# Performance work log

Hardware: AMD Instinct MI355X
Metric: run time of the kernel (lower is better)

Reference implementation:

```python
import jax, jax.numpy as jnp
import numpy as np

C = 512
NH = 8
HD = C // NH              # head dim = 64
TOPK = int(HD * 2 / 3)    # keep top-2/3 entries per attention row (DRSformer-style)


def conv2d(x, w, b, groups=1, pad=0):
    y = jax.lax.conv_general_dilated(
        x, w, window_strides=(1, 1), padding=[(pad, pad), (pad, pad)],
        dimension_numbers=('NCHW', 'OIHW', 'NCHW'), feature_group_count=groups)
    return y + b[None, :, None, None]


def setup_inputs() -> dict:
    key = jax.random.key(0)
    ks = jax.random.split(key, 8)
    s = lambda k, sh, fan: jax.random.normal(k, sh, jnp.float32) * (1.0 / np.sqrt(fan))
    return {
        'x': jax.random.normal(ks[0], (2, C, 128, 128), jnp.float32),
        'w_qkv': s(ks[1], (3 * C, C, 1, 1), C),          # 1x1 conv C -> 3C
        'b_qkv': jnp.zeros((3 * C,), jnp.float32),
        'w_dw': s(ks[2], (3 * C, 1, 3, 3), 9),           # 3x3 depthwise on 3C
        'b_dw': jnp.zeros((3 * C,), jnp.float32),
        'scale': jnp.asarray(HD ** -0.5, jnp.float32),   # learned scalar temperature
        'w_proj': s(ks[3], (C, C, 1, 1), C),             # output 1x1 conv
        'b_proj': jnp.zeros((C,), jnp.float32),
    }


def reference(x, w_qkv, b_qkv, w_dw, b_dw, scale, w_proj, b_proj):
    B, _, H, W = x.shape
    # qkv generator: 1x1 conv then 3x3 depthwise conv (Restormer-style)
    qkv = conv2d(x, w_qkv, b_qkv)
    qkv = conv2d(qkv, w_dw, b_dw, groups=3 * C, pad=1)
    q, k, v = jnp.split(qkv, 3, axis=1)
    # b (nh c) h w -> b nh c (h w)
    rs = lambda t: t.reshape(B, NH, HD, H * W)
    q, k, v = rs(q), rs(k), rs(v)
    # L2-normalize along spatial (token) dim
    q = q / jnp.maximum(jnp.linalg.norm(q, axis=-1, keepdims=True), 1e-12)
    k = k / jnp.maximum(jnp.linalg.norm(k, axis=-1, keepdims=True), 1e-12)
    # transposed (channel) attention: [B, NH, HD, HD]
    att = jnp.einsum('bhcn,bhdn->bhcd', q, k) * scale
    # sparsify: keep top-k per row, mask rest to -inf, then softmax
    thresh = jax.lax.top_k(att, TOPK)[0][..., -1:]
    att = jnp.where(att >= thresh, att, -jnp.inf)
    att = jax.nn.softmax(att, axis=-1)
    out = jnp.einsum('bhcd,bhdn->bhcn', att, v)  # [B, NH, HD, HW]
    out = out.reshape(B, C, H, W)
    return conv2d(out, w_proj, b_proj)
```

## Files before the change

### kernel.cpp

```cpp
#include <hip/hip_runtime.h>

typedef unsigned short u16;
typedef _Float16 f16x8 __attribute__((ext_vector_type(8)));
typedef u16 u16x8 __attribute__((ext_vector_type(8)));
typedef u16 u16x4 __attribute__((ext_vector_type(4)));
typedef float f32x4 __attribute__((ext_vector_type(4)));

#define NTOK 16384
#define CCH 512
#define SXN ((long)CCH * NTOK)

__device__ __forceinline__ float h2f(u16 u) {
  _Float16 h = *(_Float16*)&u; return (float)h;
}
__device__ __forceinline__ u16 f2h(float f) {
  _Float16 h = (_Float16)f; return *(u16*)&h;
}
__device__ __forceinline__ void split2(float v, u16& hi, u16& lo) {
  hi = f2h(v); lo = f2h(v - h2f(hi));
}
__device__ __forceinline__ int swz(int row, int ko) { return ko ^ ((row & 7) << 3); }

__device__ __forceinline__ int k2swz(int r, int x) {
  int s = x >> 2, e = x & 3;
  int ps = (((s >> 2) + r) & 7) | ((s & 3) << 3);
  return r * 128 + (ps << 2) + e;
}

__global__ __launch_bounds__(256) void k0_transpose(
    const float* __restrict__ x, u16* __restrict__ xh) {
  __shared__ float ld[64][65];
  const int t = threadIdx.x;
  const int n0 = blockIdx.x * 64, c0 = blockIdx.y * 64;
#pragma unroll
  for (int j = 0; j < 4; ++j) {
    int idx = t + 256 * j;
    int cl = idx >> 4, ns = (idx & 15) * 4;
    float4 v = *(const float4*)(x + (long)(c0 + cl) * NTOK + n0 + ns);
    ld[cl][ns] = v.x; ld[cl][ns + 1] = v.y; ld[cl][ns + 2] = v.z; ld[cl][ns + 3] = v.w;
  }
  __syncthreads();
#pragma unroll
  for (int j = 0; j < 4; ++j) {
    int idx = t + 256 * j;
    int nl = idx >> 4, cs = (idx & 15) * 4;
    u16x4 h;
#pragma unroll
    for (int e = 0; e < 4; ++e) h[e] = f2h(ld[cs + e][nl]);
    *(u16x4*)(xh + (long)(n0 + nl) * CCH + c0 + cs) = h;
  }
}

__global__ __launch_bounds__(256) void k0_cvt_w(const float* __restrict__ a,
                                                u16* __restrict__ oh,
                                                u16* __restrict__ ol) {
  int i = blockIdx.x * 256 + threadIdx.x;
  const float4 v = ((const float4*)a)[i];
  u16 h0, l0, h1, l1, h2, l2, h3, l3;
  split2(v.x, h0, l0); split2(v.y, h1, l1);
  split2(v.z, h2, l2); split2(v.w, h3, l3);
  ((unsigned long long*)oh)[i] = (unsigned long long)h0 | ((unsigned long long)h1 << 16)
                               | ((unsigned long long)h2 << 32) | ((unsigned long long)h3 << 48);
  ((unsigned long long*)ol)[i] = (unsigned long long)l0 | ((unsigned long long)l1 << 16)
                               | ((unsigned long long)l2 << 32) | ((unsigned long long)l3 << 48);
}

__device__ __forceinline__ void storeC(u16* p, float v) { *p = f2h(v); }
__device__ __forceinline__ void storeC(float* p, float v) { *p = v; }

template <typename OutT, bool BIAS_ROW, int GRP, bool GRP_IS_M>
__global__ __launch_bounds__(256) void gemm_bt(
    const u16* __restrict__ A, const u16* __restrict__ B, OutT* __restrict__ C,
    const float* __restrict__ bias, int ldc) {
  const int K = 512;
  __shared__ __align__(16) u16 lA[128 * 64];
  __shared__ __align__(16) u16 lB[128 * 64];
  const int t = threadIdx.x;
  const int lane = t & 63, w = t >> 6;
  const int wm = w & 1, wn = w >> 1;
  const int fx = blockIdx.x, fy = blockIdx.y;
  const int gg = fy & (GRP - 1);
  const int go = fx + 8 * (fy / GRP);
  const int bm = (GRP_IS_M ? gg : go) * 128;
  const int bn = (GRP_IS_M ? go : gg) * 128;
  const f32x4 zero4 = {0.f, 0.f, 0.f, 0.f};
  f32x4 acc[4][4];
#pragma unroll
  for (int i = 0; i < 4; ++i)
#pragma unroll
    for (int j = 0; j < 4; ++j) acc[i][j] = zero4;

  for (int kt = 0; kt < K; kt += 64) {
    u16x8 ra[4], rb[4];
#pragma unroll
    for (int j = 0; j < 4; ++j) {
      int idx = t + 256 * j;
      int row = idx >> 3, ko = (idx & 7) << 3;
      ra[j] = *(const u16x8*)(A + (long)(bm + row) * K + kt + ko);
      rb[j] = *(const u16x8*)(B + (long)(bn + row) * K + kt + ko);
    }
    __syncthreads();
#pragma unroll
    for (int j = 0; j < 4; ++j) {
      int idx = t + 256 * j;
      int row = idx >> 3, ko = (idx & 7) << 3;
      *(u16x8*)(&lA[row * 64 + swz(row, ko)]) = ra[j];
      *(u16x8*)(&lB[row * 64 + swz(row, ko)]) = rb[j];
    }
    __syncthreads();
#pragma unroll
    for (int kk = 0; kk < 2; ++kk) {
      f16x8 af[4], bfr[4];
#pragma unroll
      for (int f = 0; f < 4; ++f) {
        int ar = wm * 64 + f * 16 + (lane & 15);
        int br = wn * 64 + f * 16 + (lane & 15);
        int ko = kk * 32 + (lane >> 4) * 8;
        af[f]  = *(const f16x8*)(&lA[ar * 64 + swz(ar, ko)]);
        bfr[f] = *(const f16x8*)(&lB[br * 64 + swz(br, ko)]);
      }
#pragma unroll
      for (int i = 0; i < 4; ++i)
#pragma unroll
        for (int jj = 0; jj < 4; ++jj)
          acc[i][jj] = __builtin_amdgcn_mfma_f32_16x16x32_f16(af[i], bfr[jj], acc[i][jj], 0, 0, 0);
    }
  }
#pragma unroll
  for (int i = 0; i < 4; ++i) {
    const int r0 = bm + wm * 64 + i * 16 + (lane >> 4) * 4;
#pragma unroll
    for (int jj = 0; jj < 4; ++jj) {
      const int c0 = bn + wn * 64 + jj * 16 + (lane & 15);
      const float bcol = BIAS_ROW ? 0.f : bias[c0];
#pragma unroll
      for (int r = 0; r < 4; ++r) {
        float v = acc[i][jj][r] + (BIAS_ROW ? bias[r0 + r] : bcol);
        storeC(&C[(long)(r0 + r) * ldc + c0], v);
      }
    }
  }
}

__global__ __launch_bounds__(256) void gemm_split(
    const u16* __restrict__ Ah, const u16* __restrict__ Al,
    const u16* __restrict__ Bh,
    u16* __restrict__ C, const float* __restrict__ bias, int ldc) {
  const int K = 512;
  __shared__ __align__(16) u16 lAh[128 * 64];
  __shared__ __align__(16) u16 lBh[128 * 64];
  const int t = threadIdx.x;
  const int lane = t & 63, w = t >> 6;
  const int wm = w & 1, wn = w >> 1;
  const int fx = blockIdx.x, fy = blockIdx.y;
  const int bm = (fy & 7) * 128;
  const int bn = (fx + ((fy >> 3) << 3)) * 128;
  const f32x4 zero4 = {0.f, 0.f, 0.f, 0.f};
  f32x4 acc[4][4];
#pragma unroll
  for (int i = 0; i < 4; ++i)
#pragma unroll
    for (int j = 0; j < 4; ++j) acc[i][j] = zero4;

  const u16* Alp = Al + (long)(bm + wm * 64 + (lane & 15)) * K + ((lane >> 4) << 3);

  for (int kt = 0; kt < K; kt += 64) {
    u16x8 rah[4], rbh[4];
#pragma unroll
    for (int j = 0; j < 4; ++j) {
      int idx = t + 256 * j;
      int row = idx >> 3, ko = (idx & 7) << 3;
      rah[j] = *(const u16x8*)(Ah + (long)(bm + row) * K + kt + ko);
      rbh[j] = *(const u16x8*)(Bh + (long)(bn + row) * K + kt + ko);
    }
    f16x8 afl[2][4];
#pragma unroll
    for (int kk = 0; kk < 2; ++kk)
#pragma unroll
      for (int f = 0; f < 4; ++f)
        afl[kk][f] = *(const f16x8*)(Alp + (long)(f * 16) * K + kt + kk * 32);
    __syncthreads();
#pragma unroll
    for (int j = 0; j < 4; ++j) {
      int idx = t + 256 * j;
      int row = idx >> 3, ko = (idx & 7) << 3;
      *(u16x8*)(&lAh[row * 64 + swz(row, ko)]) = rah[j];
      *(u16x8*)(&lBh[row * 64 + swz(row, ko)]) = rbh[j];
    }
    __syncthreads();
#pragma unroll
    for (int kk = 0; kk < 2; ++kk) {
      f16x8 afh[4], bfh[4];
#pragma unroll
      for (int f = 0; f < 4; ++f) {
        int ar = wm * 64 + f * 16 + (lane & 15);
        int br = wn * 64 + f * 16 + (lane & 15);
        int ko = kk * 32 + (lane >> 4) * 8;
        afh[f] = *(const f16x8*)(&lAh[ar * 64 + swz(ar, ko)]);
        bfh[f] = *(const f16x8*)(&lBh[br * 64 + swz(br, ko)]);
      }
#pragma unroll
      for (int i = 0; i < 4; ++i)
#pragma unroll
        for (int jj = 0; jj < 4; ++jj) {
          acc[i][jj] = __builtin_amdgcn_mfma_f32_16x16x32_f16(afh[i], bfh[jj], acc[i][jj], 0, 0, 0);
          acc[i][jj] = __builtin_amdgcn_mfma_f32_16x16x32_f16(afl[kk][i], bfh[jj], acc[i][jj], 0, 0, 0);
        }
    }
  }
#pragma unroll
  for (int i = 0; i < 4; ++i) {
    const int r0 = bm + wm * 64 + i * 16 + (lane >> 4) * 4;
#pragma unroll
    for (int jj = 0; jj < 4; ++jj) {
      const int c0 = bn + wn * 64 + jj * 16 + (lane & 15);
#pragma unroll
      for (int r = 0; r < 4; ++r) {
        C[(long)(r0 + r) * ldc + c0] = f2h(acc[i][jj][r] + bias[r0 + r]);
      }
    }
  }
}

__global__ __launch_bounds__(256) void k2_qk(
    const u16* __restrict__ qkpre,
    const float* __restrict__ wdw, const float* __restrict__ bdw,
    u16* __restrict__ qh, u16* __restrict__ kh, float* __restrict__ sumsq) {
  __shared__ float st[34 * 128];
  const int t = threadIdx.x;
  const int s = blockIdx.x;
  const int ch = blockIdx.y;
  const int y0 = s * 32;
  const u16* src = qkpre + (long)ch * NTOK;
  for (int i = t; i < 1088; i += 256) {
    int r = i >> 5, sl = i & 31;
    int gy = y0 - 1 + r;
    float4 v = {0.f, 0.f, 0.f, 0.f};
    if (gy >= 0 && gy < 128) {
      u16x4 h4 = *(const u16x4*)(src + gy * 128 + sl * 4);
      v.x = h2f(h4[0]); v.y = h2f(h4[1]); v.z = h2f(h4[2]); v.w = h2f(h4[3]);
    }
    *(float4*)(&st[k2swz(r, sl * 4)]) = v;
  }
  float wv[9];
#pragma unroll
  for (int i = 0; i < 9; ++i) wv[i] = wdw[ch * 9 + i];
  const float bi = bdw[ch];
  __syncthreads();
  const int y = t >> 3, xg = t & 7, x16 = xg * 16;
  float r0[18], r1[18], r2[18];
#pragma unroll
  for (int k = 0; k < 4; ++k) {
    *(float4*)(&r0[1 + 4 * k]) = *(const float4*)(&st[k2swz(y + 0, x16 + 4 * k)]);
    *(float4*)(&r1[1 + 4 * k]) = *(const float4*)(&st[k2swz(y + 1, x16 + 4 * k)]);
    *(float4*)(&r2[1 + 4 * k]) = *(const float4*)(&st[k2swz(y + 2, x16 + 4 * k)]);
  }
  r0[0]  = (xg > 0) ? st[k2swz(y + 0, x16 - 1)] : 0.f;
  r1[0]  = (xg > 0) ? st[k2swz(y + 1, x16 - 1)] : 0.f;
  r2[0]  = (xg > 0) ? st[k2swz(y + 2, x16 - 1)] : 0.f;
  r0[17] = (xg < 7) ? st[k2swz(y + 0, x16 + 16)] : 0.f;
  r1[17] = (xg < 7) ? st[k2swz(y + 1, x16 + 16)] : 0.f;
  r2[17] = (xg < 7) ? st[k2swz(y + 2, x16 + 16)] : 0.f;
  u16 oh[16];
  float ss = 0.f;
#pragma unroll
  for (int j = 0; j < 16; ++j) {
    float o = bi;
    o += wv[0] * r0[j] + wv[1] * r0[j + 1] + wv[2] * r0[j + 2];
    o += wv[3] * r1[j] + wv[4] * r1[j + 1] + wv[5] * r1[j + 2];
    o += wv[6] * r2[j] + wv[7] * r2[j + 1] + wv[8] * r2[j + 2];
    ss += o * o;
    oh[j] = f2h(o);
  }
  const bool isq = ch < 512;
  u16* dh = isq ? qh : kh;
  const long o = (long)(isq ? ch : ch - 512) * NTOK + (y0 + y) * 128 + x16;
  *(u16x8*)(dh + o)     = *(u16x8*)&oh[0];
  *(u16x8*)(dh + o + 8) = *(u16x8*)&oh[8];
#pragma unroll
  for (int off = 32; off > 0; off >>= 1) ss += __shfl_xor(ss, off);
  if ((t & 63) == 0) atomicAdd(&sumsq[ch], ss);
}

__global__ __launch_bounds__(256) void k2_v(
    const u16* __restrict__ vpre, const float* __restrict__ wdw,
    const float* __restrict__ bdw, u16* __restrict__ vtm) {
  __shared__ __align__(16) u16 st[3 * 66 * 64];
  const int t = threadIdx.x;
  const int xc = blockIdx.x & 1, cc = blockIdx.x >> 1;
  const int y = blockIdx.y;
  const int c0 = cc * 64;
  for (int i = t; i < 1584; i += 256) {
    int l8 = i & 7, dyxi = i >> 3;
    int dy = dyxi / 66, xi = dyxi - dy * 66;
    int yy = y + dy - 1, xx = xc * 64 + xi - 1;
    u16x8 val = {0, 0, 0, 0, 0, 0, 0, 0};
    if (yy >= 0 && yy < 128 && xx >= 0 && xx < 128)
      val = *(const u16x8*)(vpre + (long)(yy * 128 + xx) * 512 + c0 + l8 * 8);
    *(u16x8*)(&st[dyxi * 64 + l8 * 8]) = val;
  }
  __syncthreads();
  const int ch2 = t & 31;
  const int xq = t >> 5;
  const int cga = 1024 + c0 + 2 * ch2;
  float w0[9], w1[9];
#pragma unroll
  for (int i = 0; i < 9; ++i) { w0[i] = wdw[cga * 9 + i]; w1[i] = wdw[(cga + 1) * 9 + i]; }
  const float bi0 = bdw[cga], bi1 = bdw[cga + 1];
  const int nb = y * 128 + xc * 64;
#pragma unroll
  for (int m = 0; m < 8; ++m) {
    int xl = xq * 8 + m;
    float s0 = bi0, s1 = bi1;
#pragma unroll
    for (int dy = 0; dy < 3; ++dy)
#pragma unroll
      for (int dx = 0; dx < 3; ++dx) {
        unsigned int v2 = *(const unsigned int*)(&st[(dy * 66 + xl + dx) * 64 + 2 * ch2]);
        s0 += w0[dy * 3 + dx] * h2f((u16)(v2 & 0xffffu));
        s1 += w1[dy * 3 + dx] * h2f((u16)(v2 >> 16));
      }
    unsigned int pack = (unsigned int)f2h(s0) | ((unsigned int)f2h(s1) << 16);
    *(unsigned int*)(vtm + (long)(nb + xq * 8 + m) * 512 + c0 + 2 * ch2) = pack;
  }
}

__global__ __launch_bounds__(256) void k3_qk(
    const u16* __restrict__ qh, const u16* __restrict__ kh,
    float* __restrict__ att_raw) {
  __shared__ __align__(16) u16 lq[64 * 128];
  __shared__ __align__(16) u16 lk[64 * 128];
  const int t = threadIdx.x, lane = t & 63, w = t >> 6;
  const int h = blockIdx.y;
  const int n0b = blockIdx.x * 256;
  const u16* qhb = qh + (long)(h * 64) * NTOK;
  const u16* khb = kh + (long)(h * 64) * NTOK;
  const f32x4 zero4 = {0.f, 0.f, 0.f, 0.f};
  f32x4 acc[4] = {zero4, zero4, zero4, zero4};
  for (int ch = 0; ch < 2; ++ch) {
    const int n0 = n0b + ch * 128;
    u16x8 r0[4], r2[4];
#pragma unroll
    for (int j = 0; j < 4; ++j) {
      int idx = t + 256 * j;
      int row = idx >> 4, ko = (idx & 15) << 3;
      long o = (long)row * NTOK + n0 + ko;
      r0[j] = *(const u16x8*)(qhb + o);
      r2[j] = *(const u16x8*)(khb + o);
    }
    __syncthreads();
#pragma unroll
    for (int j = 0; j < 4; ++j) {
      int idx = t + 256 * j;
      int row = idx >> 4, ko = (idx & 15) << 3;
      int sko = swz(row, ko);
      *(u16x8*)(&lq[row * 128 + sko]) = r0[j];
      *(u16x8*)(&lk[row * 128 + sko]) = r2[j];
    }
    __syncthreads();
#pragma unroll
    for (int kk = 0; kk < 4; ++kk) {
      int br = w * 16 + (lane & 15);
      int ko = kk * 32 + (lane >> 4) * 8;
      f16x8 bfh = *(const f16x8*)(&lk[br * 128 + swz(br, ko)]);
#pragma unroll
      for (int f = 0; f < 4; ++f) {
        int ar = f * 16 + (lane & 15);
        f16x8 afh = *(const f16x8*)(&lq[ar * 128 + swz(ar, ko)]);
        acc[f] = __builtin_amdgcn_mfma_f32_16x16x32_f16(afh, bfh, acc[f], 0, 0, 0);
      }
    }
  }
  float* dst = att_raw + h * 64 * 64;
#pragma unroll
  for (int f = 0; f < 4; ++f) {
    int rr = f * 16 + (lane >> 4) * 4;
    int col = w * 16 + (lane & 15);
#pragma unroll
    for (int r = 0; r < 4; ++r) atomicAdd(&dst[(rr + r) * 64 + col], acc[f][r]);
  }
}

__global__ __launch_bounds__(256) void k4_sm(const float* __restrict__ att_raw,
                                             const float* __restrict__ sumsq,
                                             const float* __restrict__ scale_p,
                                             float* __restrict__ att) {
  const int t = threadIdx.x, lane = t & 63, w = t >> 6;
  const int row = blockIdx.x * 4 + w;
  const int hi = row >> 6, i = row & 63;
  const float scale = scale_p[0];
  const float nq = fmaxf(sqrtf(sumsq[hi * 64 + i]), 1e-12f);
  const float nk = fmaxf(sqrtf(sumsq[512 + hi * 64 + lane]), 1e-12f);
  float v = att_raw[(long)row * 64 + lane] * scale / (nq * nk);
  int cnt = 0;
  for (int m = 0; m < 64; ++m) {
    float vm = __shfl(v, m);
    cnt += (vm > v || (vm == v && m < lane)) ? 1 : 0;
  }
  unsigned long long ball = __ballot(cnt == 41);
  float thresh = __shfl(v, (int)__builtin_ctzll(ball));
  bool keep = v >= thresh;
  float mx = v;
#pragma unroll
  for (int o = 32; o > 0; o >>= 1) mx = fmaxf(mx, __shfl_xor(mx, o));
  float e = keep ? __expf(v - mx) : 0.f;
  float s = e;
#pragma unroll
  for (int o = 32; o > 0; o >>= 1) s += __shfl_xor(s, o);
  att[(long)row * 64 + lane] = e / s;
}

__global__ __launch_bounds__(256) void k4b_m(const float* __restrict__ att,
                                             const float* __restrict__ wproj,
                                             u16* __restrict__ Mb) {
  __shared__ float wl[64][68];
  __shared__ float al[64][64];
  const int t = threadIdx.x;
  const int cb = blockIdx.x, h = blockIdx.y;
  const int c0 = cb * 64;
#pragma unroll
  for (int j = 0; j < 4; ++j) {
    int idx = t + 256 * j;
    int r = idx >> 4, c4 = (idx & 15) * 4;
    *(float4*)(&wl[r][c4]) = *(const float4*)(&wproj[(long)(c0 + r) * 512 + h * 64 + c4]);
    *(float4*)(&al[r][c4]) = *(const float4*)(&att[(h * 64 + r) * 64 + c4]);
  }
  __syncthreads();
  const int jd4 = (t & 15) * 4, r0 = t >> 4;
  f32x4 acc[4];
  const f32x4 zero4 = {0.f, 0.f, 0.f, 0.f};
#pragma unroll
  for (int m = 0; m < 4; ++m) acc[m] = zero4;
#pragma unroll
  for (int i2 = 0; i2 < 64; ++i2) {
    f32x4 a4 = *(const f32x4*)(&al[i2][jd4]);
#pragma unroll
    for (int m = 0; m < 4; ++m) {
      float wv = wl[r0 + m * 16][i2];
      acc[m] += wv * a4;
    }
  }
#pragma unroll
  for (int m = 0; m < 4; ++m) {
    u16x4 p;
#pragma unroll
    for (int e = 0; e < 4; ++e) p[e] = f2h(acc[m][e]);
    *(u16x4*)(Mb + (long)(c0 + r0 + m * 16) * 512 + h * 64 + jd4) = p;
  }
}

extern "C" void kernel_launch(void* const* d_in, const int* in_sizes, int n_in,
                              void* d_out, int out_size, void* d_ws, size_t ws_size,
                              hipStream_t stream) {
  (void)in_sizes; (void)n_in; (void)out_size; (void)ws_size;
  const float* x      = (const float*)d_in[0];
  const float* w_qkv  = (const float*)d_in[1];
  const float* b_qkv  = (const float*)d_in[2];
  const float* w_dw   = (const float*)d_in[3];
  const float* b_dw   = (const float*)d_in[4];
  const float* scale  = (const float*)d_in[5];
  const float* w_proj = (const float*)d_in[6];
  const float* b_proj = (const float*)d_in[7];
  float* out = (float*)d_out;
  char* ws = (char*)d_ws;

  u16* qkpre16  = (u16*)(ws + 0L);
  u16* xT_hi    = (u16*)(ws + 67108864L);
  u16* k_hi     = (u16*)(ws + 100663296L);
  u16* vpre     = (u16*)(ws + 134217728L);
  u16* vtm      = (u16*)(ws + 150994944L);
  u16* whi      = (u16*)(ws + 167772160L);
  u16* wlo      = (u16*)(ws + 169345024L);
  float* sumsq  = (float*)(ws + 170917888L);
  float* att_raw= (float*)(ws + 170921984L);
  float* att    = (float*)(ws + 171053056L);
  u16* Mb       = (u16*)(ws + 171184128L);
  u16* q_hi = xT_hi;

  k0_cvt_w<<<dim3(768), 256, 0, stream>>>(w_qkv, whi, wlo);

  for (int b = 0; b < 2; ++b) {
    const float* xb = x + (long)b * SXN;
    float* outb = out + (long)b * SXN;

    hipMemsetAsync(sumsq, 0, 4096 + 131072, stream);
    k0_transpose<<<dim3(256, 8, 1), 256, 0, stream>>>(xb, xT_hi);
    gemm_split<<<dim3(8, 128, 1), 256, 0, stream>>>(
        whi, wlo, xT_hi, qkpre16, b_qkv, NTOK);
    gemm_bt<u16, false, 4, false><<<dim3(8, 64, 1), 256, 0, stream>>>(
        xT_hi, whi + (long)1024 * 512, vpre, b_qkv + 1024, 512);
    k2_qk<<<dim3(4, 1024, 1), 256, 0, stream>>>(
        qkpre16, w_dw, b_dw, q_hi, k_hi, sumsq);
    k2_v<<<dim3(16, 128, 1), 256, 0, stream>>>(vpre, w_dw, b_dw, vtm);
    k3_qk<<<dim3(64, 8, 1), 256, 0, stream>>>(q_hi, k_hi, att_raw);
    k4_sm<<<dim3(128), 256, 0, stream>>>(att_raw, sumsq, scale, att);
    k4b_m<<<dim3(8, 8, 1), 256, 0, stream>>>(att, w_proj, Mb);
    gemm_bt<float, true, 4, true><<<dim3(8, 64, 1), 256, 0, stream>>>(
        Mb, vtm, outb, b_proj, NTOK);
  }
}
```

Before: 304.0 us.

## Batch both images into each kernel launch via blockIdx.z

Replaces the per-batch host loop with single launches that cover both batch elements through a z grid dimension and per-batch strides, and sizes the workspace buffers for two batches. Vpre is staged in the output buffer to fit the workspace. The aim is to halve launch count and double the grid of the small kernels (softmax, att·wproj, qk gram) so the GPU is fuller. It costs a larger workspace footprint and relies on the output buffer being free before the final GEMM writes it.

```diff
diff --git a/kernel.cpp b/kernel.cpp
--- a/kernel.cpp
+++ b/kernel.cpp
@@ -9,6 +9,10 @@
 #define NTOK 16384
 #define CCH 512
 #define SXN ((long)CCH * NTOK)
+#define SQK (512L * NTOK)
+#define SQP (1024L * NTOK)
+#define SAR 32768L
+#define SMB (512L * 512)
 
 __device__ __forceinline__ float h2f(u16 u) {
   _Float16 h = *(_Float16*)&u; return (float)h;
@@ -30,6 +34,8 @@
 __global__ __launch_bounds__(256) void k0_transpose(
     const float* __restrict__ x, u16* __restrict__ xh) {
   __shared__ float ld[64][65];
+  const long bz = blockIdx.z;
+  x += bz * SXN; xh += bz * SQK;
   const int t = threadIdx.x;
   const int n0 = blockIdx.x * 64, c0 = blockIdx.y * 64;
 #pragma unroll
@@ -71,10 +77,12 @@
 template <typename OutT, bool BIAS_ROW, int GRP, bool GRP_IS_M>
 __global__ __launch_bounds__(256) void gemm_bt(
     const u16* __restrict__ A, const u16* __restrict__ B, OutT* __restrict__ C,
-    const float* __restrict__ bias, int ldc) {
+    const float* __restrict__ bias, int ldc, long sA, long sB, long sC) {
   const int K = 512;
   __shared__ __align__(16) u16 lA[128 * 64];
   __shared__ __align__(16) u16 lB[128 * 64];
+  const long bz = blockIdx.z;
+  A += bz * sA; B += bz * sB; C += bz * sC;
   const int t = threadIdx.x;
   const int lane = t & 63, w = t >> 6;
   const int wm = w & 1, wn = w >> 1;
@@ -149,6 +157,8 @@
   const int K = 512;
   __shared__ __align__(16) u16 lAh[128 * 64];
   __shared__ __align__(16) u16 lBh[128 * 64];
+  const long bz = blockIdx.z;
+  Bh += bz * SQK; C += bz * SQP;
   const int t = threadIdx.x;
   const int lane = t & 63, w = t >> 6;
   const int wm = w & 1, wn = w >> 1;
@@ -227,6 +237,8 @@
     const float* __restrict__ wdw, const float* __restrict__ bdw,
     u16* __restrict__ qh, u16* __restrict__ kh, float* __restrict__ sumsq) {
   __shared__ float st[34 * 128];
+  const long bz = blockIdx.z;
+  qkpre += bz * SQP; qh += bz * SQK; kh += bz * SQK; sumsq += bz * 1024;
   const int t = threadIdx.x;
   const int s = blockIdx.x;
   const int ch = blockIdx.y;
@@ -286,6 +298,8 @@
     const u16* __restrict__ vpre, const float* __restrict__ wdw,
     const float* __restrict__ bdw, u16* __restrict__ vtm) {
   __shared__ __align__(16) u16 st[3 * 66 * 64];
+  const long bz = blockIdx.z;
+  vpre += bz * SQK; vtm += bz * SQK;
   const int t = threadIdx.x;
   const int xc = blockIdx.x & 1, cc = blockIdx.x >> 1;
   const int y = blockIdx.y;
@@ -330,6 +344,8 @@
     float* __restrict__ att_raw) {
   __shared__ __align__(16) u16 lq[64 * 128];
   __shared__ __align__(16) u16 lk[64 * 128];
+  const long bz = blockIdx.z;
+  qh += bz * SQK; kh += bz * SQK; att_raw += bz * SAR;
   const int t = threadIdx.x, lane = t & 63, w = t >> 6;
   const int h = blockIdx.y;
   const int n0b = blockIdx.x * 256;
@@ -385,6 +401,8 @@
                                              const float* __restrict__ sumsq,
                                              const float* __restrict__ scale_p,
                                              float* __restrict__ att) {
+  const long bz = blockIdx.z;
+  att_raw += bz * SAR; sumsq += bz * 1024; att += bz * SAR;
   const int t = threadIdx.x, lane = t & 63, w = t >> 6;
   const int row = blockIdx.x * 4 + w;
   const int hi = row >> 6, i = row & 63;
@@ -415,6 +433,8 @@
                                              u16* __restrict__ Mb) {
   __shared__ float wl[64][68];
   __shared__ float al[64][64];
+  const long bz = blockIdx.z;
+  att += bz * SAR; Mb += bz * SMB;
   const int t = threadIdx.x;
   const int cb = blockIdx.x, h = blockIdx.y;
   const int c0 = cb * 64;
@@ -467,35 +487,31 @@
   u16* qkpre16  = (u16*)(ws + 0L);
   u16* xT_hi    = (u16*)(ws + 67108864L);
   u16* k_hi     = (u16*)(ws + 100663296L);
-  u16* vpre     = (u16*)(ws + 134217728L);
-  u16* vtm      = (u16*)(ws + 150994944L);
+  u16* vtm      = (u16*)(ws + 134217728L);
   u16* whi      = (u16*)(ws + 167772160L);
   u16* wlo      = (u16*)(ws + 169345024L);
   float* sumsq  = (float*)(ws + 170917888L);
-  float* att_raw= (float*)(ws + 170921984L);
-  float* att    = (float*)(ws + 171053056L);
-  u16* Mb       = (u16*)(ws + 171184128L);
+  float* att_raw= (float*)(ws + 170926080L);
+  float* att    = (float*)(ws + 171188224L);
+  u16* Mb       = (u16*)(ws + 171450368L);
   u16* q_hi = xT_hi;
+  u16* vpre = (u16*)d_out;
 
   k0_cvt_w<<<dim3(768), 256, 0, stream>>>(w_qkv, whi, wlo);
-
-  for (int b = 0; b < 2; ++b) {
-    const float* xb = x + (long)b * SXN;
-    float* outb = out + (long)b * SXN;
-
-    hipMemsetAsync(sumsq, 0, 4096 + 131072, stream);
-    k0_transpose<<<dim3(256, 8, 1), 256, 0, stream>>>(xb, xT_hi);
-    gemm_split<<<dim3(8, 128, 1), 256, 0, stream>>>(
-        whi, wlo, xT_hi, qkpre16, b_qkv, NTOK);
-    gemm_bt<u16, false, 4, false><<<dim3(8, 64, 1), 256, 0, stream>>>(
-        xT_hi, whi + (long)1024 * 512, vpre, b_qkv + 1024, 512);
-    k2_qk<<<dim3(4, 1024, 1), 256, 0, stream>>>(
-        qkpre16, w_dw, b_dw, q_hi, k_hi, sumsq);
-    k2_v<<<dim3(16, 128, 1), 256, 0, stream>>>(vpre, w_dw, b_dw, vtm);
-    k3_qk<<<dim3(64, 8, 1), 256, 0, stream>>>(q_hi, k_hi, att_raw);
-    k4_sm<<<dim3(128), 256, 0, stream>>>(att_raw, sumsq, scale, att);
-    k4b_m<<<dim3(8, 8, 1), 256, 0, stream>>>(att, w_proj, Mb);
-    gemm_bt<float, true, 4, true><<<dim3(8, 64, 1), 256, 0, stream>>>(
-        Mb, vtm, outb, b_proj, NTOK);
-  }
-}
+  hipMemsetAsync(sumsq, 0, 8192 + 262144, stream);
+
+  k0_transpose<<<dim3(256, 8, 2), 256, 0, stream>>>(x, xT_hi);
+  gemm_split<<<dim3(8, 128, 2), 256, 0, stream>>>(
+      whi, wlo, xT_hi, qkpre16, b_qkv, NTOK);
+  gemm_bt<u16, false, 4, false><<<dim3(8, 64, 2), 256, 0, stream>>>(
+      xT_hi, whi + (long)1024 * 512, vpre, b_qkv + 1024, 512,
+      SQK, 0L, SQK);
+  k2_qk<<<dim3(4, 1024, 2), 256, 0, stream>>>(
+      qkpre16, w_dw, b_dw, q_hi, k_hi, sumsq);
+  k2_v<<<dim3(16, 128, 2), 256, 0, stream>>>(vpre, w_dw, b_dw, vtm);
+  k3_qk<<<dim3(64, 8, 2), 256, 0, stream>>>(q_hi, k_hi, att_raw);
+  k4_sm<<<dim3(128, 1, 2), 256, 0, stream>>>(att_raw, sumsq, scale, att);
+  k4b_m<<<dim3(8, 8, 2), 256, 0, stream>>>(att, w_proj, Mb);
+  gemm_bt<float, true, 4, true><<<dim3(8, 64, 2), 256, 0, stream>>>(
+      Mb, vtm, out, b_proj, NTOK, SMB, SQK, SXN);
+}
```

Measured after the change: 262.5 us (median of 3 runs). 1.16x faster.
